# Optimization experiments

Hardware: AMD Instinct MI355X
Metric: run time of the kernel (lower is better)

The kernel has to match this reference:

```python
import jax, jax.numpy as jnp
import numpy as np

B, Z, C, H, W = 512, 256, 3, 64, 64
DATASET_SIZE = 737280
LOG2PI = float(np.log(2.0 * np.pi))


def setup_inputs() -> dict:
    key = jax.random.key(0)
    k1, k2, k3, k4, k5 = jax.random.split(key, 5)
    # pixel data / reconstructions in (0,1) for bernoulli BCE (avoid log(0))
    data = jax.random.uniform(k1, (B, C, H, W), dtype=jnp.float32) * 0.98 + 0.01
    recon_batch = jax.random.uniform(k2, (B, C, H, W), dtype=jnp.float32) * 0.98 + 0.01
    latent_sample = jax.random.normal(k3, (B, Z), dtype=jnp.float32)
    mu = jax.random.normal(k4, (B, Z), dtype=jnp.float32) * 0.1
    logvar = jax.random.normal(k5, (B, Z), dtype=jnp.float32) * 0.1
    return {"data": data, "recon_batch": recon_batch, "latent_sample": latent_sample,
            "mu": mu, "logvar": logvar, "dataset_size": DATASET_SIZE}


def _log_density_normal(sample, mu, logvar):
    # NOTE: faithful to source: inv_var = exp(logvar) (repo quirk, not exp(-logvar))
    return -0.5 * ((sample - mu) ** 2 * jnp.exp(logvar) + logvar + LOG2PI)


def reference(data, recon_batch, latent_sample, mu, logvar, dataset_size):
    bsz = data.shape[0]
    # bernoulli reconstruction loss (BCE summed, normalized per batch)
    rec_loss = -jnp.sum(data * jnp.log(recon_batch)
                        + (1.0 - data) * jnp.log(1.0 - recon_batch)) / bsz
    # dimension-wise KL (faithful to source: exp(logvar + mu^2))
    dw_kl_loss = jnp.mean(jnp.sum(-0.5 * logvar
                                  + 0.5 * jnp.exp(logvar + mu ** 2) - 0.5, axis=1))
    # pairwise log q(z_i | x_j): [B, B, Z]
    logqz_mat = _log_density_normal(latent_sample[:, None, :],
                                    mu[None, :, :], logvar[None, :, :])
    log_norm = float(np.log(bsz)) + jnp.log(jnp.asarray(dataset_size, jnp.float32))
    # sum_k [ logsumexp_j logq(i,j,k) - log(B*N) ]
    logqz_prodmarginals = jnp.sum(jax.nn.logsumexp(logqz_mat, axis=1) - log_norm, axis=1)
    # logsumexp_j sum_k logq(i,j,k) - log(B*N)
    logqz = jax.nn.logsumexp(jnp.sum(logqz_mat, axis=2), axis=1) - log_norm
    tc_loss = jnp.mean(logqz - logqz_prodmarginals)
    elbo = rec_loss + tc_loss + dw_kl_loss
    return elbo
```

## Files before the change

### kernel.cpp

```cpp
#include <hip/hip_runtime.h>

#define BATCH 512
#define ZDIM 256


__device__ __forceinline__ float fast_exp2(float x) {
#if __has_builtin(__builtin_amdgcn_exp2f)
    return __builtin_amdgcn_exp2f(x);
#else
    return exp2f(x);
#endif
}

__device__ __forceinline__ float wave_reduce_sum(float v) {
#pragma unroll
    for (int off = 32; off > 0; off >>= 1)
        v += __shfl_down(v, off, 64);
    return v;
}

__device__ __forceinline__ float wave_reduce_max(float v) {
#pragma unroll
    for (int off = 32; off > 0; off >>= 1)
        v = fmaxf(v, __shfl_down(v, off, 64));
    return v;
}

__device__ __forceinline__ float block_sum256(float v, float* red) {
    float w = wave_reduce_sum(v);
    if ((threadIdx.x & 63) == 0) red[threadIdx.x >> 6] = w;
    __syncthreads();
    float r = red[0] + red[1] + red[2] + red[3];
    __syncthreads();
    return r;
}


__global__ __launch_bounds__(256) void k_tables(
    const float* __restrict__ mu, const float* __restrict__ logvar,
    float4* __restrict__ abc, float2* __restrict__ e2wT2,
    float* __restrict__ cj, float* __restrict__ dwrow,
    unsigned int* __restrict__ cnt) {
    __shared__ float red[4];
    int j = blockIdx.x, k = threadIdx.x;
    if (j == 0 && k == 0) cnt[0] = 0u;
    float m = mu[j * ZDIM + k];
    float lv = logvar[j * ZDIM + k];
    float ev = __expf(lv);
    float e2n = -0.5f * ev;
    float lcn = -0.5f * (lv + 1.8378770664093453f);
    const float L2E = 1.4426950408889634f;
    float cpart = m * m * e2n + lcn;
    abc[j * ZDIM + k] = make_float4(e2n * L2E, m * ev * L2E, cpart * L2E, 0.f);
    e2wT2[(((k >> 1) * BATCH + j) << 1) + (k & 1)] = make_float2(e2n, m * ev);
    float csum = block_sum256(cpart, red);
    if (k == 0) cj[j] = csum;
    float dw = -0.5f * lv + 0.5f * __expf(lv + m * m) - 0.5f;
    float dsum = block_sum256(dw, red);
    if (k == 0) dwrow[j] = dsum;
}

__global__ __launch_bounds__(256) void k_bulk(
    const float4* __restrict__ d, const float4* __restrict__ r,
    const float* __restrict__ lat, const float4* __restrict__ abc,
    float* __restrict__ part,
    const float4* __restrict__ e2wT2, const float* __restrict__ cj,
    float* __restrict__ smat, float* __restrict__ recpart) {
    __shared__ float ss[8 * ZDIM];
    int b = blockIdx.x, t = threadIdx.x;
    if (b < 128) {
        int i0 = (b >> 1) * 8;
        int j = (b & 1) * 256 + t;
#pragma unroll
        for (int li = 0; li < 8; li++)
            ss[t * 8 + li] = lat[(i0 + li) * ZDIM + t];
        __syncthreads();
        float acc[8];
#pragma unroll
        for (int i = 0; i < 8; i++) acc[i] = 0.f;
#pragma unroll 4
        for (int k2 = 0; k2 < ZDIM / 2; k2++) {
            float4 ew = e2wT2[k2 * BATCH + j];
            const float4* sp = (const float4*)(ss + (2 * k2) * 8);
            float4 sa = sp[0], sb = sp[1];
            float4 sc = sp[2], sd = sp[3];
            acc[0] = fmaf(sa.x, fmaf(sa.x, ew.x, ew.y), acc[0]);
            acc[1] = fmaf(sa.y, fmaf(sa.y, ew.x, ew.y), acc[1]);
            acc[2] = fmaf(sa.z, fmaf(sa.z, ew.x, ew.y), acc[2]);
            acc[3] = fmaf(sa.w, fmaf(sa.w, ew.x, ew.y), acc[3]);
            acc[4] = fmaf(sb.x, fmaf(sb.x, ew.x, ew.y), acc[4]);
            acc[5] = fmaf(sb.y, fmaf(sb.y, ew.x, ew.y), acc[5]);
            acc[6] = fmaf(sb.z, fmaf(sb.z, ew.x, ew.y), acc[6]);
            acc[7] = fmaf(sb.w, fmaf(sb.w, ew.x, ew.y), acc[7]);
            acc[0] = fmaf(sc.x, fmaf(sc.x, ew.z, ew.w), acc[0]);
            acc[1] = fmaf(sc.y, fmaf(sc.y, ew.z, ew.w), acc[1]);
            acc[2] = fmaf(sc.z, fmaf(sc.z, ew.z, ew.w), acc[2]);
            acc[3] = fmaf(sc.w, fmaf(sc.w, ew.z, ew.w), acc[3]);
            acc[4] = fmaf(sd.x, fmaf(sd.x, ew.z, ew.w), acc[4]);
            acc[5] = fmaf(sd.y, fmaf(sd.y, ew.z, ew.w), acc[5]);
            acc[6] = fmaf(sd.z, fmaf(sd.z, ew.z, ew.w), acc[6]);
            acc[7] = fmaf(sd.w, fmaf(sd.w, ew.z, ew.w), acc[7]);
        }
        float c = cj[j];
#pragma unroll
        for (int i = 0; i < 8; i++)
            smat[(i0 + i) * BATCH + j] = acc[i] + c;
    } else if (b < 640) {
        int pb = b - 128;
        int i0 = (pb >> 3) * 8, j0 = (pb & 7) * 64;
        float s[8], s2[8], a[8];
#pragma unroll
        for (int i = 0; i < 8; i++) {
            s[i] = lat[(i0 + i) * ZDIM + t];
            s2[i] = s[i] * s[i];
            a[i] = 0.f;
        }
        for (int j2 = 0; j2 < 16; j2++) {
            int j = j0 + j2 * 4;
            float4 q0 = abc[(j + 0) * ZDIM + t];
            float4 q1 = abc[(j + 1) * ZDIM + t];
            float4 q2 = abc[(j + 2) * ZDIM + t];
            float4 q3 = abc[(j + 3) * ZDIM + t];
#pragma unroll
            for (int i = 0; i < 8; i++) {
                a[i] += fast_exp2(fmaf(s2[i], q0.x, fmaf(s[i], q0.y, q0.z)));
                a[i] += fast_exp2(fmaf(s2[i], q1.x, fmaf(s[i], q1.y, q1.z)));
                a[i] += fast_exp2(fmaf(s2[i], q2.x, fmaf(s[i], q2.y, q2.z)));
                a[i] += fast_exp2(fmaf(s2[i], q3.x, fmaf(s[i], q3.y, q3.z)));
            }
        }
#pragma unroll
        for (int i = 0; i < 8; i++)
            part[((pb & 7) * BATCH + i0 + i) * ZDIM + t] = a[i];
    } else {
        int rb = b - 640;
        float s = 0.f;
        int base = rb * 256 + t;
#pragma unroll 4
        for (int it = 0; it < 12; ++it) {
            int idx = base + it * 131072;
            float4 dv = d[idx];
            float4 rv = r[idx];
            s += dv.x * __logf(rv.x) + (1.f - dv.x) * __logf(1.f - rv.x);
            s += dv.y * __logf(rv.y) + (1.f - dv.y) * __logf(1.f - rv.y);
            s += dv.z * __logf(rv.z) + (1.f - dv.z) * __logf(1.f - rv.z);
            s += dv.w * __logf(rv.w) + (1.f - dv.w) * __logf(1.f - rv.w);
        }
        float tot = block_sum256(s, ss);
        if (t == 0) recpart[rb] = tot;
    }
}

__global__ __launch_bounds__(256) void k_finalize(
    const float* __restrict__ part, const float* __restrict__ smat,
    const int* __restrict__ dsz, const float* __restrict__ recpart,
    const float* __restrict__ dwrow, float* __restrict__ tcpart,
    unsigned int* __restrict__ cnt, float* __restrict__ out) {
    __shared__ float red[4];
    int i = blockIdx.x, t = threadIdx.x;
    float s = 0.f;
#pragma unroll
    for (int jc = 0; jc < 8; jc++)
        s += part[(jc * BATCH + i) * ZDIM + t];
    float prod_i = block_sum256(__logf(s), red);
    float v1 = smat[i * BATCH + t];
    float v2 = smat[i * BATCH + 256 + t];
    float m = wave_reduce_max(fmaxf(v1, v2));
    if ((t & 63) == 0) red[t >> 6] = m;
    __syncthreads();
    m = fmaxf(fmaxf(red[0], red[1]), fmaxf(red[2], red[3]));
    __syncthreads();
    float e = __expf(v1 - m) + __expf(v2 - m);
    float sum = block_sum256(e, red);
    __shared__ bool amLast;
    if (t == 0) {
        float log_norm = __logf(512.f) + __logf((float)dsz[0]);
        float logqz = m + __logf(sum) - log_norm;
        float pm = prod_i - 256.f * log_norm;
        __hip_atomic_store(&tcpart[i], logqz - pm, __ATOMIC_RELAXED,
                           __HIP_MEMORY_SCOPE_AGENT);
        unsigned int old = __hip_atomic_fetch_add(cnt, 1u, __ATOMIC_ACQ_REL,
                                                  __HIP_MEMORY_SCOPE_AGENT);
        amLast = (old == BATCH - 1);
    }
    __syncthreads();
    if (amLast) {
        float acc = 0.f;
        float tc1 = __hip_atomic_load(&tcpart[t], __ATOMIC_RELAXED,
                                      __HIP_MEMORY_SCOPE_AGENT);
        float tc2 = __hip_atomic_load(&tcpart[t + 256], __ATOMIC_RELAXED,
                                      __HIP_MEMORY_SCOPE_AGENT);
        acc += tc1 + tc2;
        acc += dwrow[t] + dwrow[t + 256];
        acc -= recpart[t] + recpart[t + 256];
        float tot = block_sum256(acc, red);
        if (t == 0) out[0] = tot * (1.f / 512.f);
    }
}


extern "C" void kernel_launch(void* const* d_in, const int* in_sizes, int n_in,
                              void* d_out, int out_size, void* d_ws, size_t ws_size,
                              hipStream_t stream) {
    const float* data   = (const float*)d_in[0];
    const float* recon  = (const float*)d_in[1];
    const float* lat    = (const float*)d_in[2];
    const float* mu     = (const float*)d_in[3];
    const float* logvar = (const float*)d_in[4];
    const int*   dsz    = (const int*)d_in[5];
    float* out = (float*)d_out;

    float*  ws      = (float*)d_ws;
    unsigned int* cnt = (unsigned int*)ws;
    float*  recpart = ws + 64;
    float*  dwrow   = recpart + 512;
    float*  tcpart  = dwrow + 512;
    float*  cj      = tcpart + 512;
    float4* abc     = (float4*)(ws + 4096);
    float*  e2wT2   = ws + 4096 + 524288;
    float*  part    = ws + 4096 + 786432;
    float*  smat    = part + 1048576;

    k_tables<<<512, 256, 0, stream>>>(mu, logvar, abc, (float2*)e2wT2,
                                      cj, dwrow, cnt);
    k_bulk<<<1152, 256, 0, stream>>>((const float4*)data, (const float4*)recon,
                                     lat, abc, part, (const float4*)e2wT2,
                                     cj, smat, recpart);
    k_finalize<<<512, 256, 0, stream>>>(part, smat, dsz, recpart, dwrow,
                                        tcpart, cnt, out);
}
```

Before: 121.0 us.

## Fuse three kernels into one persistent megakernel with atomic-counter grid barriers

Merges the table, bulk and finalize kernels into one launch of 1152 blocks. Blocks synchronise through atomic counters with spin-waits instead of kernel boundaries, so the BCE blocks can overlap the table stage. This removes two kernel launch gaps and the drains between them. In exchange it adds a memset, spin-wait overhead, and a deadlock risk if not all 1152 blocks can be resident at once (launch_bounds 256,5 is meant to allow this).

```diff
diff --git a/kernel.cpp b/kernel.cpp
--- a/kernel.cpp
+++ b/kernel.cpp
@@ -35,105 +35,131 @@
     return r;
 }
 
-
-__global__ __launch_bounds__(256) void k_tables(
+__device__ __forceinline__ void release_count(unsigned int* c) {
+    __syncthreads();
+    if (threadIdx.x == 0)
+        __hip_atomic_fetch_add(c, 1u, __ATOMIC_RELEASE, __HIP_MEMORY_SCOPE_AGENT);
+}
+
+__device__ __forceinline__ void acquire_count(unsigned int* c, unsigned int tgt) {
+    if (threadIdx.x == 0) {
+        while (__hip_atomic_load(c, __ATOMIC_ACQUIRE, __HIP_MEMORY_SCOPE_AGENT) < tgt)
+            __builtin_amdgcn_s_sleep(2);
+    }
+    __syncthreads();
+}
+
+__global__ __launch_bounds__(256, 5) void k_mega(
+    const float4* __restrict__ d, const float4* __restrict__ r,
+    const float* __restrict__ lat,
     const float* __restrict__ mu, const float* __restrict__ logvar,
+    const int* __restrict__ dsz,
     float4* __restrict__ abc, float2* __restrict__ e2wT2,
     float* __restrict__ cj, float* __restrict__ dwrow,
-    unsigned int* __restrict__ cnt) {
+    float* __restrict__ recpart, float* __restrict__ part,
+    float* __restrict__ smat, float* __restrict__ tcpart,
+    unsigned int* __restrict__ cnts, float* __restrict__ out) {
+    __shared__ float ss[8 * ZDIM];
     __shared__ float red[4];
-    int j = blockIdx.x, k = threadIdx.x;
-    if (j == 0 && k == 0) cnt[0] = 0u;
-    float m = mu[j * ZDIM + k];
-    float lv = logvar[j * ZDIM + k];
-    float ev = __expf(lv);
-    float e2n = -0.5f * ev;
-    float lcn = -0.5f * (lv + 1.8378770664093453f);
-    const float L2E = 1.4426950408889634f;
-    float cpart = m * m * e2n + lcn;
-    abc[j * ZDIM + k] = make_float4(e2n * L2E, m * ev * L2E, cpart * L2E, 0.f);
-    e2wT2[(((k >> 1) * BATCH + j) << 1) + (k & 1)] = make_float2(e2n, m * ev);
-    float csum = block_sum256(cpart, red);
-    if (k == 0) cj[j] = csum;
-    float dw = -0.5f * lv + 0.5f * __expf(lv + m * m) - 0.5f;
-    float dsum = block_sum256(dw, red);
-    if (k == 0) dwrow[j] = dsum;
-}
-
-__global__ __launch_bounds__(256) void k_bulk(
-    const float4* __restrict__ d, const float4* __restrict__ r,
-    const float* __restrict__ lat, const float4* __restrict__ abc,
-    float* __restrict__ part,
-    const float4* __restrict__ e2wT2, const float* __restrict__ cj,
-    float* __restrict__ smat, float* __restrict__ recpart) {
-    __shared__ float ss[8 * ZDIM];
     int b = blockIdx.x, t = threadIdx.x;
-    if (b < 128) {
-        int i0 = (b >> 1) * 8;
-        int j = (b & 1) * 256 + t;
-#pragma unroll
-        for (int li = 0; li < 8; li++)
-            ss[t * 8 + li] = lat[(i0 + li) * ZDIM + t];
-        __syncthreads();
-        float acc[8];
-#pragma unroll
-        for (int i = 0; i < 8; i++) acc[i] = 0.f;
-#pragma unroll 4
-        for (int k2 = 0; k2 < ZDIM / 2; k2++) {
-            float4 ew = e2wT2[k2 * BATCH + j];
-            const float4* sp = (const float4*)(ss + (2 * k2) * 8);
-            float4 sa = sp[0], sb = sp[1];
-            float4 sc = sp[2], sd = sp[3];
-            acc[0] = fmaf(sa.x, fmaf(sa.x, ew.x, ew.y), acc[0]);
-            acc[1] = fmaf(sa.y, fmaf(sa.y, ew.x, ew.y), acc[1]);
-            acc[2] = fmaf(sa.z, fmaf(sa.z, ew.x, ew.y), acc[2]);
-            acc[3] = fmaf(sa.w, fmaf(sa.w, ew.x, ew.y), acc[3]);
-            acc[4] = fmaf(sb.x, fmaf(sb.x, ew.x, ew.y), acc[4]);
-            acc[5] = fmaf(sb.y, fmaf(sb.y, ew.x, ew.y), acc[5]);
-            acc[6] = fmaf(sb.z, fmaf(sb.z, ew.x, ew.y), acc[6]);
-            acc[7] = fmaf(sb.w, fmaf(sb.w, ew.x, ew.y), acc[7]);
-            acc[0] = fmaf(sc.x, fmaf(sc.x, ew.z, ew.w), acc[0]);
-            acc[1] = fmaf(sc.y, fmaf(sc.y, ew.z, ew.w), acc[1]);
-            acc[2] = fmaf(sc.z, fmaf(sc.z, ew.z, ew.w), acc[2]);
-            acc[3] = fmaf(sc.w, fmaf(sc.w, ew.z, ew.w), acc[3]);
-            acc[4] = fmaf(sd.x, fmaf(sd.x, ew.z, ew.w), acc[4]);
-            acc[5] = fmaf(sd.y, fmaf(sd.y, ew.z, ew.w), acc[5]);
-            acc[6] = fmaf(sd.z, fmaf(sd.z, ew.z, ew.w), acc[6]);
-            acc[7] = fmaf(sd.w, fmaf(sd.w, ew.z, ew.w), acc[7]);
-        }
-        float c = cj[j];
-#pragma unroll
-        for (int i = 0; i < 8; i++)
-            smat[(i0 + i) * BATCH + j] = acc[i] + c;
-    } else if (b < 640) {
-        int pb = b - 128;
-        int i0 = (pb >> 3) * 8, j0 = (pb & 7) * 64;
-        float s[8], s2[8], a[8];
-#pragma unroll
-        for (int i = 0; i < 8; i++) {
-            s[i] = lat[(i0 + i) * ZDIM + t];
-            s2[i] = s[i] * s[i];
-            a[i] = 0.f;
-        }
-        for (int j2 = 0; j2 < 16; j2++) {
-            int j = j0 + j2 * 4;
-            float4 q0 = abc[(j + 0) * ZDIM + t];
-            float4 q1 = abc[(j + 1) * ZDIM + t];
-            float4 q2 = abc[(j + 2) * ZDIM + t];
-            float4 q3 = abc[(j + 3) * ZDIM + t];
+    unsigned int* tcnt = cnts + 0;
+    unsigned int* pcnt = cnts + 1;
+    unsigned int* cnt3 = cnts + 2;
+
+    if (b < 512) {
+        {
+            int j = b, k = t;
+            float m = mu[j * ZDIM + k];
+            float lv = logvar[j * ZDIM + k];
+            float ev = __expf(lv);
+            float e2n = -0.5f * ev;
+            float lcn = -0.5f * (lv + 1.8378770664093453f);
+            const float L2E = 1.4426950408889634f;
+            float cpart = m * m * e2n + lcn;
+            abc[j * ZDIM + k] = make_float4(e2n * L2E, m * ev * L2E,
+                                            cpart * L2E, 0.f);
+            e2wT2[(((k >> 1) * BATCH + j) << 1) + (k & 1)] =
+                make_float2(e2n, m * ev);
+            float csum = block_sum256(cpart, red);
+            if (k == 0) cj[j] = csum;
+            float dw = -0.5f * lv + 0.5f * __expf(lv + m * m) - 0.5f;
+            float dsum = block_sum256(dw, red);
+            if (k == 0) dwrow[j] = dsum;
+        }
+        release_count(tcnt);
+        acquire_count(tcnt, 512u);
+        {
+            int i0 = (b >> 3) * 8, j0 = (b & 7) * 64;
+            float s[8], s2[8], a[8];
 #pragma unroll
             for (int i = 0; i < 8; i++) {
-                a[i] += fast_exp2(fmaf(s2[i], q0.x, fmaf(s[i], q0.y, q0.z)));
-                a[i] += fast_exp2(fmaf(s2[i], q1.x, fmaf(s[i], q1.y, q1.z)));
-                a[i] += fast_exp2(fmaf(s2[i], q2.x, fmaf(s[i], q2.y, q2.z)));
-                a[i] += fast_exp2(fmaf(s2[i], q3.x, fmaf(s[i], q3.y, q3.z)));
-            }
-        }
-#pragma unroll
-        for (int i = 0; i < 8; i++)
-            part[((pb & 7) * BATCH + i0 + i) * ZDIM + t] = a[i];
-    } else {
-        int rb = b - 640;
+                s[i] = lat[(i0 + i) * ZDIM + t];
+                s2[i] = s[i] * s[i];
+                a[i] = 0.f;
+            }
+            for (int j2 = 0; j2 < 16; j2++) {
+                int j = j0 + j2 * 4;
+                float4 q0 = abc[(j + 0) * ZDIM + t];
+                float4 q1 = abc[(j + 1) * ZDIM + t];
+                float4 q2 = abc[(j + 2) * ZDIM + t];
+                float4 q3 = abc[(j + 3) * ZDIM + t];
+#pragma unroll
+                for (int i = 0; i < 8; i++) {
+                    a[i] += fast_exp2(fmaf(s2[i], q0.x, fmaf(s[i], q0.y, q0.z)));
+                    a[i] += fast_exp2(fmaf(s2[i], q1.x, fmaf(s[i], q1.y, q1.z)));
+                    a[i] += fast_exp2(fmaf(s2[i], q2.x, fmaf(s[i], q2.y, q2.z)));
+                    a[i] += fast_exp2(fmaf(s2[i], q3.x, fmaf(s[i], q3.y, q3.z)));
+                }
+            }
+#pragma unroll
+            for (int i = 0; i < 8; i++)
+                part[((b & 7) * BATCH + i0 + i) * ZDIM + t] = a[i];
+        }
+        release_count(pcnt);
+        acquire_count(pcnt, 1152u);
+        {
+            int i = b;
+            float s = 0.f;
+#pragma unroll
+            for (int jc = 0; jc < 8; jc++)
+                s += part[(jc * BATCH + i) * ZDIM + t];
+            float prod_i = block_sum256(__logf(s), red);
+            float v1 = smat[i * BATCH + t];
+            float v2 = smat[i * BATCH + 256 + t];
+            float m = wave_reduce_max(fmaxf(v1, v2));
+            if ((t & 63) == 0) red[t >> 6] = m;
+            __syncthreads();
+            m = fmaxf(fmaxf(red[0], red[1]), fmaxf(red[2], red[3]));
+            __syncthreads();
+            float e = __expf(v1 - m) + __expf(v2 - m);
+            float sum = block_sum256(e, red);
+            __shared__ bool amLast;
+            if (t == 0) {
+                float log_norm = __logf(512.f) + __logf((float)dsz[0]);
+                float logqz = m + __logf(sum) - log_norm;
+                float pm = prod_i - 256.f * log_norm;
+                __hip_atomic_store(&tcpart[i], logqz - pm, __ATOMIC_RELAXED,
+                                   __HIP_MEMORY_SCOPE_AGENT);
+                unsigned int old = __hip_atomic_fetch_add(
+                    cnt3, 1u, __ATOMIC_ACQ_REL, __HIP_MEMORY_SCOPE_AGENT);
+                amLast = (old == BATCH - 1);
+            }
+            __syncthreads();
+            if (amLast) {
+                float acc = 0.f;
+                float tc1 = __hip_atomic_load(&tcpart[t], __ATOMIC_RELAXED,
+                                              __HIP_MEMORY_SCOPE_AGENT);
+                float tc2 = __hip_atomic_load(&tcpart[t + 256], __ATOMIC_RELAXED,
+                                              __HIP_MEMORY_SCOPE_AGENT);
+                acc += tc1 + tc2;
+                acc += dwrow[t] + dwrow[t + 256];
+                acc -= recpart[t] + recpart[t + 256];
+                float tot = block_sum256(acc, red);
+                if (t == 0) out[0] = tot * (1.f / 512.f);
+            }
+        }
+    } else if (b < 1024) {
+        int rb = b - 512;
         float s = 0.f;
         int base = rb * 256 + t;
 #pragma unroll 4
@@ -146,55 +172,50 @@
             s += dv.z * __logf(rv.z) + (1.f - dv.z) * __logf(1.f - rv.z);
             s += dv.w * __logf(rv.w) + (1.f - dv.w) * __logf(1.f - rv.w);
         }
-        float tot = block_sum256(s, ss);
+        float tot = block_sum256(s, red);
         if (t == 0) recpart[rb] = tot;
-    }
-}
-
-__global__ __launch_bounds__(256) void k_finalize(
-    const float* __restrict__ part, const float* __restrict__ smat,
-    const int* __restrict__ dsz, const float* __restrict__ recpart,
-    const float* __restrict__ dwrow, float* __restrict__ tcpart,
-    unsigned int* __restrict__ cnt, float* __restrict__ out) {
-    __shared__ float red[4];
-    int i = blockIdx.x, t = threadIdx.x;
-    float s = 0.f;
-#pragma unroll
-    for (int jc = 0; jc < 8; jc++)
-        s += part[(jc * BATCH + i) * ZDIM + t];
-    float prod_i = block_sum256(__logf(s), red);
-    float v1 = smat[i * BATCH + t];
-    float v2 = smat[i * BATCH + 256 + t];
-    float m = wave_reduce_max(fmaxf(v1, v2));
-    if ((t & 63) == 0) red[t >> 6] = m;
-    __syncthreads();
-    m = fmaxf(fmaxf(red[0], red[1]), fmaxf(red[2], red[3]));
-    __syncthreads();
-    float e = __expf(v1 - m) + __expf(v2 - m);
-    float sum = block_sum256(e, red);
-    __shared__ bool amLast;
-    if (t == 0) {
-        float log_norm = __logf(512.f) + __logf((float)dsz[0]);
-        float logqz = m + __logf(sum) - log_norm;
-        float pm = prod_i - 256.f * log_norm;
-        __hip_atomic_store(&tcpart[i], logqz - pm, __ATOMIC_RELAXED,
-                           __HIP_MEMORY_SCOPE_AGENT);
-        unsigned int old = __hip_atomic_fetch_add(cnt, 1u, __ATOMIC_ACQ_REL,
-                                                  __HIP_MEMORY_SCOPE_AGENT);
-        amLast = (old == BATCH - 1);
-    }
-    __syncthreads();
-    if (amLast) {
-        float acc = 0.f;
-        float tc1 = __hip_atomic_load(&tcpart[t], __ATOMIC_RELAXED,
-                                      __HIP_MEMORY_SCOPE_AGENT);
-        float tc2 = __hip_atomic_load(&tcpart[t + 256], __ATOMIC_RELAXED,
-                                      __HIP_MEMORY_SCOPE_AGENT);
-        acc += tc1 + tc2;
-        acc += dwrow[t] + dwrow[t + 256];
-        acc -= recpart[t] + recpart[t + 256];
-        float tot = block_sum256(acc, red);
-        if (t == 0) out[0] = tot * (1.f / 512.f);
+        release_count(pcnt);
+    } else {
+        acquire_count(tcnt, 512u);
+        int sb = b - 1024;
+        int i0 = (sb >> 1) * 8;
+        int j = (sb & 1) * 256 + t;
+#pragma unroll
+        for (int li = 0; li < 8; li++)
+            ss[t * 8 + li] = lat[(i0 + li) * ZDIM + t];
+        __syncthreads();
+        float acc[8];
+#pragma unroll
+        for (int i = 0; i < 8; i++) acc[i] = 0.f;
+        const float4* e2w4 = (const float4*)e2wT2;
+#pragma unroll 4
+        for (int k2 = 0; k2 < ZDIM / 2; k2++) {
+            float4 ew = e2w4[k2 * BATCH + j];
+            const float4* sp = (const float4*)(ss + (2 * k2) * 8);
+            float4 sa = sp[0], sb2 = sp[1];
+            float4 sc = sp[2], sd = sp[3];
+            acc[0] = fmaf(sa.x, fmaf(sa.x, ew.x, ew.y), acc[0]);
+            acc[1] = fmaf(sa.y, fmaf(sa.y, ew.x, ew.y), acc[1]);
+            acc[2] = fmaf(sa.z, fmaf(sa.z, ew.x, ew.y), acc[2]);
+            acc[3] = fmaf(sa.w, fmaf(sa.w, ew.x, ew.y), acc[3]);
+            acc[4] = fmaf(sb2.x, fmaf(sb2.x, ew.x, ew.y), acc[4]);
+            acc[5] = fmaf(sb2.y, fmaf(sb2.y, ew.x, ew.y), acc[5]);
+            acc[6] = fmaf(sb2.z, fmaf(sb2.z, ew.x, ew.y), acc[6]);
+            acc[7] = fmaf(sb2.w, fmaf(sb2.w, ew.x, ew.y), acc[7]);
+            acc[0] = fmaf(sc.x, fmaf(sc.x, ew.z, ew.w), acc[0]);
+            acc[1] = fmaf(sc.y, fmaf(sc.y, ew.z, ew.w), acc[1]);
+            acc[2] = fmaf(sc.z, fmaf(sc.z, ew.z, ew.w), acc[2]);
+            acc[3] = fmaf(sc.w, fmaf(sc.w, ew.z, ew.w), acc[3]);
+            acc[4] = fmaf(sd.x, fmaf(sd.x, ew.z, ew.w), acc[4]);
+            acc[5] = fmaf(sd.y, fmaf(sd.y, ew.z, ew.w), acc[5]);
+            acc[6] = fmaf(sd.z, fmaf(sd.z, ew.z, ew.w), acc[6]);
+            acc[7] = fmaf(sd.w, fmaf(sd.w, ew.z, ew.w), acc[7]);
+        }
+        float c = cj[j];
+#pragma unroll
+        for (int i = 0; i < 8; i++)
+            smat[(i0 + i) * BATCH + j] = acc[i] + c;
+        release_count(pcnt);
     }
 }
 
@@ -211,7 +232,7 @@
     float* out = (float*)d_out;
 
     float*  ws      = (float*)d_ws;
-    unsigned int* cnt = (unsigned int*)ws;
+    unsigned int* cnts = (unsigned int*)ws;
     float*  recpart = ws + 64;
     float*  dwrow   = recpart + 512;
     float*  tcpart  = dwrow + 512;
@@ -221,11 +242,10 @@
     float*  part    = ws + 4096 + 786432;
     float*  smat    = part + 1048576;
 
-    k_tables<<<512, 256, 0, stream>>>(mu, logvar, abc, (float2*)e2wT2,
-                                      cj, dwrow, cnt);
-    k_bulk<<<1152, 256, 0, stream>>>((const float4*)data, (const float4*)recon,
-                                     lat, abc, part, (const float4*)e2wT2,
-                                     cj, smat, recpart);
-    k_finalize<<<512, 256, 0, stream>>>(part, smat, dsz, recpart, dwrow,
-                                        tcpart, cnt, out);
-}
+    hipMemsetAsync(cnts, 0, 256, stream);
+
+    k_mega<<<1152, 256, 0, stream>>>((const float4*)data, (const float4*)recon,
+                                     lat, mu, logvar, dsz,
+                                     abc, (float2*)e2wT2, cj, dwrow,
+                                     recpart, part, smat, tcpart, cnts, out);
+}
```

Result: slower. 360.3 us (+197.8%).
